# Optimization experiments

Hardware: AMD Instinct MI355X
Metric: run time of the kernel (lower is better)

Reference implementation:

```python
import jax, jax.numpy as jnp
import numpy as np

NUM_HEADS = 16
D_MODEL = 1024
NUM_LAYERS = 4
VOCAB = 32000
SEQ_LEN = 1024
BATCH = 4
EPS = 1e-6


def position_embedding(seq_len, d_model):
    pos = jnp.arange(seq_len, dtype=jnp.float32)[:, None]
    i = jnp.arange(d_model, dtype=jnp.float32)[None, :]
    # faithful to source: angle_rates = 1 / (1/10000)^(2*(i//2)/d) = 10000^(2*(i//2)/d)
    angle_rates = jnp.power(10000.0, 2.0 * jnp.floor(i / 2.0) / float(d_model))
    ang = pos * angle_rates  # [S, D]
    return jnp.concatenate([jnp.sin(ang[:, 0::2]), jnp.cos(ang[:, 1::2])], axis=-1)[None]  # [1,S,D]


def layer_norm(x, g, b):
    m = jnp.mean(x, axis=-1, keepdims=True)
    v = jnp.mean(jnp.square(x - m), axis=-1, keepdims=True)
    return (x - m) * jax.lax.rsqrt(v + EPS) * g + b


def setup_inputs() -> dict:
    key = jax.random.key(0)
    ks = jax.random.split(key, 20)
    L, D = NUM_LAYERS, D_MODEL
    s = 0.02
    inp = {
        "x": jax.random.randint(ks[0], (BATCH, SEQ_LEN), 0, VOCAB, dtype=jnp.int32),
        "mask": jnp.zeros((BATCH, 1, 1, SEQ_LEN), dtype=jnp.float32),
        "emb": jax.random.normal(ks[1], (VOCAB, D), dtype=jnp.float32) * s,
        "wq": jax.random.normal(ks[2], (L, D, D), dtype=jnp.float32) * s,
        "bq": jnp.zeros((L, D), dtype=jnp.float32),
        "wk": jax.random.normal(ks[3], (L, D, D), dtype=jnp.float32) * s,
        "bk": jnp.zeros((L, D), dtype=jnp.float32),
        "wv": jax.random.normal(ks[4], (L, D, D), dtype=jnp.float32) * s,
        "bv": jnp.zeros((L, D), dtype=jnp.float32),
        "wo": jax.random.normal(ks[5], (L, D, D), dtype=jnp.float32) * s,
        "bo": jnp.zeros((L, D), dtype=jnp.float32),
        "wf": jax.random.normal(ks[6], (L, D, D), dtype=jnp.float32) * s,
        "bf": jnp.zeros((L, D), dtype=jnp.float32),
        "g1": jnp.ones((L, D), dtype=jnp.float32),
        "b1": jnp.zeros((L, D), dtype=jnp.float32),
        "g2": jnp.ones((L, D), dtype=jnp.float32),
        "b2": jnp.zeros((L, D), dtype=jnp.float32),
    }
    return inp


def encoder_forward(x, mask, emb, wq, bq, wk, bk, wv, bv, wo, bo, wf, bf, g1, b1, g2, b2):
    B, S = x.shape
    D = emb.shape[1]
    H = NUM_HEADS
    dh = D // H
    h = emb[x] * jnp.sqrt(jnp.float32(D))  # [B,S,D]
    h = h + position_embedding(S, D)[:, :S, :]

    def split_heads(t):  # [B,S,D] -> [B,H,S,dh]
        return t.reshape(B, S, H, dh).transpose(0, 2, 1, 3)

    for l in range(wq.shape[0]):
        q = split_heads(h @ wq[l] + bq[l])
        k = split_heads(h @ wk[l] + bk[l])
        v = split_heads(h @ wv[l] + bv[l])
        scores = jnp.einsum("bhqd,bhkd->bhqk", q, k) / jnp.sqrt(jnp.float32(dh))
        scores = scores + mask * -1e9
        w = jax.nn.softmax(scores, axis=-1)
        ctx = jnp.einsum("bhqk,bhkd->bhqd", w, v)  # [B,H,S,dh]
        ctx = ctx.transpose(0, 2, 1, 3).reshape(B, S, D)
        attn_out = ctx @ wo[l] + bo[l]
        h = layer_norm(h + attn_out, g1[l], b1[l])
        ff = h @ wf[l] + bf[l]
        h = layer_norm(h + ff, g2[l], b2[l])
    return h


def reference(x, mask, emb, wq, bq, wk, bk, wv, bv, wo, bo, wf, bf, g1, b1, g2, b2):
    return encoder_forward(x, mask, emb, wq, bq, wk, bk, wv, bv, wo, bo, wf, bf, g1, b1, g2, b2)
```

## Files before the change

kernel.cpp:

```cpp
#include <hip/hip_runtime.h>
#include <hip/hip_bf16.h>
#include <math.h>

typedef __hip_bfloat16 bf16;
typedef unsigned int u32;
typedef __attribute__((ext_vector_type(8))) short short8;
typedef __attribute__((ext_vector_type(4))) float f32x4;


#define ATT_LDK 72
#define PS_LD  72

typedef __attribute__((address_space(3))) u32 lds_u32;
typedef const __attribute__((address_space(1))) u32 glb_u32;
static __device__ __forceinline__ void g2l16(const void* g, void* l) {
    __builtin_amdgcn_global_load_lds((glb_u32*)g, (lds_u32*)l, 16, 0, 0);
}

static __device__ __forceinline__ unsigned short bf16bits(float f) {
    bf16 h = __float2bfloat16(f);
    return *(unsigned short*)&h;
}

__global__ __launch_bounds__(256) void wprep_kernel(
    const float* __restrict__ wq, const float* __restrict__ wk,
    const float* __restrict__ wv, const float* __restrict__ wo,
    const float* __restrict__ wf, bf16* __restrict__ wt_all)
{
    __shared__ bf16 tile[64][ATT_LDK];
    const int z = blockIdx.z;
    const int l = z / 5, f = z % 5;
    const float* src = (f == 0) ? wq : (f == 1) ? wk : (f == 2) ? wv : (f == 3) ? wo : wf;
    src += (size_t)l * 1024 * 1024;
    bf16* dst = wt_all + ((size_t)l * 5 + f) * 1024 * 1024;

    const int k0 = blockIdx.x * 64, n0 = blockIdx.y * 64;
    const int t = threadIdx.x;
#pragma unroll
    for (int rr = 0; rr < 4; ++rr) {
        int slot = t + rr * 256;
        int r = slot >> 4, c = slot & 15;
        float4 v = *(const float4*)(src + (size_t)(k0 + r) * 1024 + n0 + c * 4);
        tile[c * 4 + 0][r] = __float2bfloat16(v.x);
        tile[c * 4 + 1][r] = __float2bfloat16(v.y);
        tile[c * 4 + 2][r] = __float2bfloat16(v.z);
        tile[c * 4 + 3][r] = __float2bfloat16(v.w);
    }
    __syncthreads();
#pragma unroll
    for (int rr = 0; rr < 2; ++rr) {
        int slot = t + rr * 256;
        int n = slot >> 3, c = slot & 7;
        *(uint4*)(dst + (size_t)(n0 + n) * 1024 + k0 + c * 8) = *(const uint4*)&tile[n][c * 8];
    }
}

__global__ void bias_stack_kernel(const float* __restrict__ bq, const float* __restrict__ bk,
                                  const float* __restrict__ bv, float* __restrict__ bqkv)
{
    int i = blockIdx.x * 256 + threadIdx.x;
    if (i < 4 * 3072) {
        int l = i / 3072, c = i % 3072;
        int fam = c >> 10, cc = c & 1023;
        const float* s = (fam == 0) ? bq : (fam == 1) ? bk : bv;
        bqkv[i] = s[l * 1024 + cc];
    }
}

__global__ __launch_bounds__(256) void pe_kernel(float* __restrict__ pe)
{
    int idx = blockIdx.x * 256 + threadIdx.x;
    int d0 = (idx & 255) * 4;
    int s = idx >> 8;
    float out[4];
#pragma unroll
    for (int j = 0; j < 4; ++j) {
        int d = d0 + j;
        int m = (d < 512) ? d : (d - 512);
        float ex = (float)(2 * m) * (1.0f / 1024.0f);
        float rate = (float)pow(10000.0, (double)ex);
        float ang = (float)s * rate;
        double a = (double)ang;
        out[j] = (d < 512) ? (float)sin(a) : (float)cos(a);
    }
    *(float4*)(pe + (size_t)s * 1024 + d0) = *(float4*)out;
}

__global__ __launch_bounds__(256) void embed_kernel(
    const int* __restrict__ x, const float* __restrict__ emb,
    const float* __restrict__ pe,
    float* __restrict__ hf, bf16* __restrict__ hb)
{
    int idx = blockIdx.x * 256 + threadIdx.x;
    int d0 = (idx & 255) * 4;
    int row = idx >> 8;
    int s = row & 1023;
    int tok = x[row];
    float4 e = *(const float4*)(emb + (size_t)tok * 1024 + d0);
    float4 p = *(const float4*)(pe + (size_t)s * 1024 + d0);
    float out[4] = {e.x * 32.0f + p.x, e.y * 32.0f + p.y,
                    e.z * 32.0f + p.z, e.w * 32.0f + p.w};
    *(float4*)(hf + (size_t)row * 1024 + d0) = *(float4*)out;
    unsigned short pk[4];
#pragma unroll
    for (int j = 0; j < 4; ++j) pk[j] = bf16bits(out[j]);
    *(uint2*)(hb + (size_t)row * 1024 + d0) = *(uint2*)pk;
}

__global__ __launch_bounds__(256, 3) void gemm_bt_kernel(
    const bf16* __restrict__ A, const bf16* __restrict__ Bt,
    const float* __restrict__ bias,
    bf16* __restrict__ Cb, bf16* __restrict__ VtOut,
    int M, int N, int K)
{
    __shared__ bf16 As[128 * 32];
    __shared__ bf16 Bs[128 * 32];
    __shared__ bf16 Cst[4][16 * PS_LD];
    const int t = threadIdx.x;
    const int lane = t & 63, wave = t >> 6;
    const int wr = wave >> 1, wc = wave & 1;
    const int lidx = lane & 15, quad = lane >> 4;
    const int m0 = blockIdx.x * 128, n0 = blockIdx.y * 128;

    f32x4 acc[4][4];
#pragma unroll
    for (int i = 0; i < 4; ++i)
#pragma unroll
        for (int j = 0; j < 4; ++j) acc[i][j] = (f32x4){0.f, 0.f, 0.f, 0.f};

    const int r0 = wave * 32;
    const int rloc = lane >> 2;
    const int csw = ((lane & 3) ^ ((lane >> 3) & 3)) * 8;
    const bf16* Abase = A  + (size_t)(m0 + r0 + rloc) * K + csw;
    const bf16* Bbase = Bt + (size_t)(n0 + r0 + rloc) * K + csw;
    bf16* AsW = As + r0 * 32;
    bf16* BsW = Bs + r0 * 32;
    const int aslot = (quad ^ ((lidx >> 1) & 3)) * 8;

    for (int k0 = 0; k0 < K; k0 += 32) {
        __syncthreads();
        g2l16(Abase + k0,                  AsW);
        g2l16(Abase + k0 + 16 * (size_t)K, AsW + 16 * 32);
        g2l16(Bbase + k0,                  BsW);
        g2l16(Bbase + k0 + 16 * (size_t)K, BsW + 16 * 32);
        __syncthreads();

        short8 af[4], bfr[4];
#pragma unroll
        for (int i = 0; i < 4; ++i)
            af[i] = *(const short8*)(As + (wr * 64 + i * 16 + lidx) * 32 + aslot);
#pragma unroll
        for (int j = 0; j < 4; ++j)
            bfr[j] = *(const short8*)(Bs + (wc * 64 + j * 16 + lidx) * 32 + aslot);
#pragma unroll
        for (int i = 0; i < 4; ++i)
#pragma unroll
            for (int j = 0; j < 4; ++j)
                acc[i][j] = __builtin_amdgcn_mfma_f32_16x16x32_bf16(af[i], bfr[j], acc[i][j], 0, 0, 0);
    }

    float bvj[4];
#pragma unroll
    for (int j = 0; j < 4; ++j)
        bvj[j] = bias ? bias[n0 + wc * 64 + j * 16 + lidx] : 0.0f;

    if (VtOut && n0 >= 2048) {
        const int bidx = m0 >> 10;
        const int s_base = (m0 & 1023) + wr * 64 + quad * 4;
        const int d_base = (n0 - 2048) + wc * 64;
#pragma unroll
        for (int i = 0; i < 4; ++i)
#pragma unroll
            for (int j = 0; j < 4; ++j) {
                unsigned short pk[4];
#pragma unroll
                for (int r = 0; r < 4; ++r)
                    pk[r] = bf16bits(acc[i][j][r] + bvj[j]);
                bf16* dst = VtOut + ((size_t)bidx * 1024 + d_base + j * 16 + lidx) * 1024
                            + s_base + i * 16;
                *(uint2*)dst = *(const uint2*)pk;
            }
    } else {
        const int row16 = lane >> 2, c4 = lane & 3;
#pragma unroll
        for (int i = 0; i < 4; ++i) {
#pragma unroll
            for (int j = 0; j < 4; ++j)
#pragma unroll
                for (int r = 0; r < 4; ++r)
                    Cst[wave][(quad * 4 + r) * PS_LD + j * 16 + lidx] =
                        __float2bfloat16(acc[i][j][r] + bvj[j]);
            bf16* dst = Cb + (size_t)(m0 + wr * 64 + i * 16 + row16) * N + n0 + wc * 64;
            const bf16* srcr = &Cst[wave][row16 * PS_LD];
#pragma unroll
            for (int h = 0; h < 2; ++h)
                *(uint4*)(dst + (c4 + 4 * h) * 8) = *(const uint4*)(srcr + (c4 + 4 * h) * 8);
        }
    }
}

__global__ __launch_bounds__(256, 4) void gemm64_kernel(
    const bf16* __restrict__ A, const bf16* __restrict__ Bt,
    const float* __restrict__ bias, float* __restrict__ Cf,
    int M, int N, int K)
{
    __shared__ bf16 As[64 * 32];
    __shared__ bf16 Bs[128 * 32];
    const int t = threadIdx.x;
    const int lane = t & 63, wave = t >> 6;
    const int wr = wave >> 1, wc = wave & 1;
    const int lidx = lane & 15, quad = lane >> 4;
    const int m0 = blockIdx.x * 64, n0 = blockIdx.y * 128;

    f32x4 acc[2][4];
#pragma unroll
    for (int i = 0; i < 2; ++i)
#pragma unroll
        for (int j = 0; j < 4; ++j) acc[i][j] = (f32x4){0.f, 0.f, 0.f, 0.f};

    const int rloc = lane >> 2;
    const int csw = ((lane & 3) ^ ((lane >> 3) & 3)) * 8;
    const bf16* Abase = A  + (size_t)(m0 + wave * 16 + rloc) * K + csw;
    const bf16* Bbase = Bt + (size_t)(n0 + wave * 32 + rloc) * K + csw;
    bf16* AsW = As + wave * 16 * 32;
    bf16* BsW = Bs + wave * 32 * 32;
    const int aslot = (quad ^ ((lidx >> 1) & 3)) * 8;

    for (int k0 = 0; k0 < K; k0 += 32) {
        __syncthreads();
        g2l16(Abase + k0,                  AsW);
        g2l16(Bbase + k0,                  BsW);
        g2l16(Bbase + k0 + 16 * (size_t)K, BsW + 16 * 32);
        __syncthreads();

        short8 af[2], bfr[4];
#pragma unroll
        for (int i = 0; i < 2; ++i)
            af[i] = *(const short8*)(As + (wr * 32 + i * 16 + lidx) * 32 + aslot);
#pragma unroll
        for (int j = 0; j < 4; ++j)
            bfr[j] = *(const short8*)(Bs + (wc * 64 + j * 16 + lidx) * 32 + aslot);
#pragma unroll
        for (int i = 0; i < 2; ++i)
#pragma unroll
            for (int j = 0; j < 4; ++j)
                acc[i][j] = __builtin_amdgcn_mfma_f32_16x16x32_bf16(af[i], bfr[j], acc[i][j], 0, 0, 0);
    }

#pragma unroll
    for (int i = 0; i < 2; ++i)
#pragma unroll
        for (int j = 0; j < 4; ++j) {
            int col = n0 + wc * 64 + j * 16 + lidx;
            float bv = bias[col];
#pragma unroll
            for (int r = 0; r < 4; ++r) {
                int rowg = m0 + wr * 32 + i * 16 + quad * 4 + r;
                Cf[(size_t)rowg * N + col] = acc[i][j][r] + bv;
            }
        }
}

__global__ __launch_bounds__(512, 4) void attention_kernel(
    const bf16* __restrict__ QKV,
    const bf16* __restrict__ Vt,
    const float* __restrict__ mask,
    bf16* __restrict__ ctx)
{
    __shared__ bf16 Ks[64 * 64];
    __shared__ bf16 Vs[64 * 64];
    __shared__ bf16 Ps[8][16 * PS_LD];

    const int t = threadIdx.x, lane = t & 63, wave = t >> 6;
    const int quad = lane >> 4, lidx = lane & 15;
    const int b = blockIdx.x >> 4, hh = blockIdx.x & 15;
    const int q0 = blockIdx.y * 128 + wave * 16;

    const int r8 = lane >> 3;
    const int gc = ((lane & 7) ^ r8) * 8;
    const bf16* kg0 = QKV + (size_t)(b * 1024 + wave * 8 + r8) * 3072 + 1024 + hh * 64 + gc;
    const bf16* vg0 = Vt  + (size_t)(b * 1024 + hh * 64 + wave * 8 + r8) * 1024 + gc;
    bf16* KsW = Ks + wave * 8 * 64;
    bf16* VsW = Vs + wave * 8 * 64;

    short8 qf[2];
    {
        const bf16* qp = QKV + (size_t)(b * 1024 + q0 + lidx) * 3072 + hh * 64;
        qf[0] = *(const short8*)(qp + quad * 8);
        qf[1] = *(const short8*)(qp + 32 + quad * 8);
    }

    f32x4 Oacc[4];
#pragma unroll
    for (int nt = 0; nt < 4; ++nt) Oacc[nt] = (f32x4){0.f, 0.f, 0.f, 0.f};
    float psum[4] = {0.f, 0.f, 0.f, 0.f};

    const int fslot = lidx & 7;

    for (int kt = 0; kt < 16; ++kt) {
        __syncthreads();
        g2l16(kg0 + (size_t)kt * 64 * 3072, KsW);
        g2l16(vg0 + kt * 64, VsW);
        __syncthreads();

        f32x4 sacc[4];
#pragma unroll
        for (int nt = 0; nt < 4; ++nt) sacc[nt] = (f32x4){0.f, 0.f, 0.f, 0.f};
#pragma unroll
        for (int kk = 0; kk < 2; ++kk)
#pragma unroll
            for (int nt = 0; nt < 4; ++nt) {
                short8 kf = *(const short8*)(Ks + (nt * 16 + lidx) * 64 + (((kk * 4 + quad) ^ fslot) * 8));
                sacc[nt] = __builtin_amdgcn_mfma_f32_16x16x32_bf16(qf[kk], kf, sacc[nt], 0, 0, 0);
            }

#pragma unroll
        for (int nt = 0; nt < 4; ++nt) {
            float mv = mask[b * 1024 + kt * 64 + nt * 16 + lidx] * -1e9f;
#pragma unroll
            for (int r = 0; r < 4; ++r) {
                float p = __expf(sacc[nt][r] * 0.125f + mv);
                sacc[nt][r] = p;
                psum[r] += p;
            }
        }

#pragma unroll
        for (int nt = 0; nt < 4; ++nt)
#pragma unroll
            for (int r = 0; r < 4; ++r)
                Ps[wave][(quad * 4 + r) * PS_LD + nt * 16 + lidx] = __float2bfloat16(sacc[nt][r]);

#pragma unroll
        for (int kk = 0; kk < 2; ++kk) {
            short8 pf = *(const short8*)(&Ps[wave][lidx * PS_LD + kk * 32 + quad * 8]);
#pragma unroll
            for (int nt = 0; nt < 4; ++nt) {
                short8 vf = *(const short8*)(Vs + (nt * 16 + lidx) * 64 + (((kk * 4 + quad) ^ fslot) * 8));
                Oacc[nt] = __builtin_amdgcn_mfma_f32_16x16x32_bf16(pf, vf, Oacc[nt], 0, 0, 0);
            }
        }
    }

#pragma unroll
    for (int off = 1; off < 16; off <<= 1)
#pragma unroll
        for (int r = 0; r < 4; ++r)
            psum[r] += __shfl_xor(psum[r], off, 64);
    float linv[4];
#pragma unroll
    for (int r = 0; r < 4; ++r) linv[r] = 1.0f / psum[r];

#pragma unroll
    for (int nt = 0; nt < 4; ++nt)
#pragma unroll
        for (int r = 0; r < 4; ++r)
            Ps[wave][(quad * 4 + r) * PS_LD + nt * 16 + lidx] = __float2bfloat16(Oacc[nt][r] * linv[r]);

    const int row16 = lane >> 2, c4 = lane & 3;
    bf16* dst = ctx + (size_t)(b * 1024 + q0 + row16) * 1024 + hh * 64;
    const bf16* srcr = &Ps[wave][row16 * PS_LD];
#pragma unroll
    for (int h = 0; h < 2; ++h)
        *(uint4*)(dst + (c4 + 4 * h) * 8) = *(const uint4*)(srcr + (c4 + 4 * h) * 8);
}

__global__ __launch_bounds__(256) void add_ln_kernel(
    const float* __restrict__ x, const float* __restrict__ dx,
    const float* __restrict__ g, const float* __restrict__ b,
    float* __restrict__ outf, bf16* __restrict__ outb)
{
    __shared__ float red[4];
    const int row = blockIdx.x;
    const int t = threadIdx.x;
    const int c0 = t * 4;
    float4 xv = *(const float4*)(x + (size_t)row * 1024 + c0);
    float4 dv = *(const float4*)(dx + (size_t)row * 1024 + c0);
    float v[4] = {xv.x + dv.x, xv.y + dv.y, xv.z + dv.z, xv.w + dv.w};
    float s = v[0] + v[1] + v[2] + v[3];
#pragma unroll
    for (int off = 1; off < 64; off <<= 1) s += __shfl_xor(s, off, 64);
    if ((t & 63) == 0) red[t >> 6] = s;
    __syncthreads();
    float mean = (red[0] + red[1] + red[2] + red[3]) * (1.0f / 1024.0f);
    float sq = 0.f;
#pragma unroll
    for (int i = 0; i < 4; ++i) { float d = v[i] - mean; sq += d * d; }
#pragma unroll
    for (int off = 1; off < 64; off <<= 1) sq += __shfl_xor(sq, off, 64);
    __syncthreads();
    if ((t & 63) == 0) red[t >> 6] = sq;
    __syncthreads();
    float var = (red[0] + red[1] + red[2] + red[3]) * (1.0f / 1024.0f);
    float rs = rsqrtf(var + 1e-6f);
    float4 gv = *(const float4*)(g + c0);
    float4 bv = *(const float4*)(b + c0);
    float gg[4] = {gv.x, gv.y, gv.z, gv.w}, bb[4] = {bv.x, bv.y, bv.z, bv.w};
    float o[4];
    unsigned short pk[4];
#pragma unroll
    for (int i = 0; i < 4; ++i) {
        o[i] = (v[i] - mean) * rs * gg[i] + bb[i];
        pk[i] = bf16bits(o[i]);
    }
    *(float4*)(outf + (size_t)row * 1024 + c0) = *(float4*)o;
    *(uint2*)(outb + (size_t)row * 1024 + c0) = *(uint2*)pk;
}

extern "C" void kernel_launch(void* const* d_in, const int* in_sizes, int n_in,
                              void* d_out, int out_size, void* d_ws, size_t ws_size,
                              hipStream_t stream)
{
    const int*   x    = (const int*)d_in[0];
    const float* mask = (const float*)d_in[1];
    const float* emb  = (const float*)d_in[2];
    const float* wq   = (const float*)d_in[3];
    const float* bq   = (const float*)d_in[4];
    const float* wk   = (const float*)d_in[5];
    const float* bk   = (const float*)d_in[6];
    const float* wv   = (const float*)d_in[7];
    const float* bv   = (const float*)d_in[8];
    const float* wo   = (const float*)d_in[9];
    const float* bo   = (const float*)d_in[10];
    const float* wf   = (const float*)d_in[11];
    const float* bfp  = (const float*)d_in[12];
    const float* g1   = (const float*)d_in[13];
    const float* b1   = (const float*)d_in[14];
    const float* g2   = (const float*)d_in[15];
    const float* b2   = (const float*)d_in[16];

    char* ws = (char*)d_ws;
    float* h_f  = (float*)ws;                 ws += 4096ull * 1024 * 4;
    bf16*  h_b  = (bf16*)ws;                  ws += 4096ull * 1024 * 2;
    bf16*  qkv  = (bf16*)ws;                  ws += 4096ull * 3072 * 2;
    bf16*  vt   = (bf16*)ws;                  ws += 4096ull * 1024 * 2;
    bf16*  ctx  = (bf16*)ws;                  ws += 4096ull * 1024 * 2;
    bf16*  wt   = (bf16*)ws;                  ws += 20ull * 1024 * 1024 * 2;
    float* pe   = (float*)ws;                 ws += 1024ull * 1024 * 4;
    float* bqkv = (float*)ws;                 ws += 4ull * 3072 * 4;
    float* delta = (float*)qkv;

    wprep_kernel<<<dim3(16, 16, 20), 256, 0, stream>>>(wq, wk, wv, wo, wf, wt);
    bias_stack_kernel<<<dim3(48), 256, 0, stream>>>(bq, bk, bv, bqkv);
    pe_kernel<<<dim3(1024), 256, 0, stream>>>(pe);
    embed_kernel<<<dim3(4096), 256, 0, stream>>>(x, emb, pe, h_f, h_b);

    for (int l = 0; l < 4; ++l) {
        bf16* wt_l = wt + (size_t)l * 5 * 1024 * 1024;
        gemm_bt_kernel<<<dim3(32, 24), 256, 0, stream>>>(
            h_b, wt_l, bqkv + l * 3072, qkv, vt, 4096, 3072, 1024);
        attention_kernel<<<dim3(64, 8), 512, 0, stream>>>(qkv, vt, mask, ctx);
        gemm64_kernel<<<dim3(64, 8), 256, 0, stream>>>(
            ctx, wt_l + 3ull * 1024 * 1024, bo + l * 1024, delta, 4096, 1024, 1024);
        add_ln_kernel<<<dim3(4096), 256, 0, stream>>>(
            h_f, delta, g1 + l * 1024, b1 + l * 1024, h_f, h_b);
        gemm64_kernel<<<dim3(64, 8), 256, 0, stream>>>(
            h_b, wt_l + 4ull * 1024 * 1024, bfp + l * 1024, delta, 4096, 1024, 1024);
        float* outf = (l == 3) ? (float*)d_out : h_f;
        add_ln_kernel<<<dim3(4096), 256, 0, stream>>>(
            h_f, delta, g2 + l * 1024, b2 + l * 1024, outf, h_b);
    }
    (void)in_sizes; (void)n_in; (void)out_size; (void)ws_size;
}
```

Before: 779.7 us.

## Double-buffer LDS tiles in GEMM and attention; fuse residual add into GEMM epilogue

The QKV GEMM, the output/FFN GEMMs and the attention kernel now keep two LDS buffers. Each iteration issues the async global-to-LDS loads for the next K tile, then computes on the current one, which halves the barriers per iteration and overlaps loads with MFMA work. Separately, gemm64 now adds the residual in its epilogue, so add_ln only reads one input. The extra LDS may lower how many attention blocks fit on a CU, and the overlap window is still closed by the barrier at the top of the next iteration.

```diff
diff --git a/kernel.cpp b/kernel.cpp
--- a/kernel.cpp
+++ b/kernel.cpp
@@ -113,8 +113,8 @@
     bf16* __restrict__ Cb, bf16* __restrict__ VtOut,
     int M, int N, int K)
 {
-    __shared__ bf16 As[128 * 32];
-    __shared__ bf16 Bs[128 * 32];
+    __shared__ bf16 As[2][128 * 32];
+    __shared__ bf16 Bs[2][128 * 32];
     __shared__ bf16 Cst[4][16 * PS_LD];
     const int t = threadIdx.x;
     const int lane = t & 63, wave = t >> 6;
@@ -133,25 +133,32 @@
     const int csw = ((lane & 3) ^ ((lane >> 3) & 3)) * 8;
     const bf16* Abase = A  + (size_t)(m0 + r0 + rloc) * K + csw;
     const bf16* Bbase = Bt + (size_t)(n0 + r0 + rloc) * K + csw;
-    bf16* AsW = As + r0 * 32;
-    bf16* BsW = Bs + r0 * 32;
+    const int lofs = r0 * 32;
     const int aslot = (quad ^ ((lidx >> 1) & 3)) * 8;
+
+    g2l16(Abase,                  &As[0][lofs]);
+    g2l16(Abase + 16 * (size_t)K, &As[0][lofs + 16 * 32]);
+    g2l16(Bbase,                  &Bs[0][lofs]);
+    g2l16(Bbase + 16 * (size_t)K, &Bs[0][lofs + 16 * 32]);
 
     for (int k0 = 0; k0 < K; k0 += 32) {
         __syncthreads();
-        g2l16(Abase + k0,                  AsW);
-        g2l16(Abase + k0 + 16 * (size_t)K, AsW + 16 * 32);
-        g2l16(Bbase + k0,                  BsW);
-        g2l16(Bbase + k0 + 16 * (size_t)K, BsW + 16 * 32);
-        __syncthreads();
+        const int cur = (k0 >> 5) & 1;
+        if (k0 + 32 < K) {
+            const int kn = k0 + 32;
+            g2l16(Abase + kn,                  &As[cur ^ 1][lofs]);
+            g2l16(Abase + kn + 16 * (size_t)K, &As[cur ^ 1][lofs + 16 * 32]);
+            g2l16(Bbase + kn,                  &Bs[cur ^ 1][lofs]);
+            g2l16(Bbase + kn + 16 * (size_t)K, &Bs[cur ^ 1][lofs + 16 * 32]);
+        }
 
         short8 af[4], bfr[4];
 #pragma unroll
         for (int i = 0; i < 4; ++i)
-            af[i] = *(const short8*)(As + (wr * 64 + i * 16 + lidx) * 32 + aslot);
+            af[i] = *(const short8*)(&As[cur][(wr * 64 + i * 16 + lidx) * 32 + aslot]);
 #pragma unroll
         for (int j = 0; j < 4; ++j)
-            bfr[j] = *(const short8*)(Bs + (wc * 64 + j * 16 + lidx) * 32 + aslot);
+            bfr[j] = *(const short8*)(&Bs[cur][(wc * 64 + j * 16 + lidx) * 32 + aslot]);
 #pragma unroll
         for (int i = 0; i < 4; ++i)
 #pragma unroll
@@ -201,11 +208,12 @@
 
 __global__ __launch_bounds__(256, 4) void gemm64_kernel(
     const bf16* __restrict__ A, const bf16* __restrict__ Bt,
-    const float* __restrict__ bias, float* __restrict__ Cf,
+    const float* __restrict__ bias, const float* __restrict__ resid,
+    float* __restrict__ Cf,
     int M, int N, int K)
 {
-    __shared__ bf16 As[64 * 32];
-    __shared__ bf16 Bs[128 * 32];
+    __shared__ bf16 As[2][64 * 32];
+    __shared__ bf16 Bs[2][128 * 32];
     const int t = threadIdx.x;
     const int lane = t & 63, wave = t >> 6;
     const int wr = wave >> 1, wc = wave & 1;
@@ -222,24 +230,31 @@
     const int csw = ((lane & 3) ^ ((lane >> 3) & 3)) * 8;
     const bf16* Abase = A  + (size_t)(m0 + wave * 16 + rloc) * K + csw;
     const bf16* Bbase = Bt + (size_t)(n0 + wave * 32 + rloc) * K + csw;
-    bf16* AsW = As + wave * 16 * 32;
-    bf16* BsW = Bs + wave * 32 * 32;
+    const int alofs = wave * 16 * 32;
+    const int blofs = wave * 32 * 32;
     const int aslot = (quad ^ ((lidx >> 1) & 3)) * 8;
+
+    g2l16(Abase,                  &As[0][alofs]);
+    g2l16(Bbase,                  &Bs[0][blofs]);
+    g2l16(Bbase + 16 * (size_t)K, &Bs[0][blofs + 16 * 32]);
 
     for (int k0 = 0; k0 < K; k0 += 32) {
         __syncthreads();
-        g2l16(Abase + k0,                  AsW);
-        g2l16(Bbase + k0,                  BsW);
-        g2l16(Bbase + k0 + 16 * (size_t)K, BsW + 16 * 32);
-        __syncthreads();
+        const int cur = (k0 >> 5) & 1;
+        if (k0 + 32 < K) {
+            const int kn = k0 + 32;
+            g2l16(Abase + kn,                  &As[cur ^ 1][alofs]);
+            g2l16(Bbase + kn,                  &Bs[cur ^ 1][blofs]);
+            g2l16(Bbase + kn + 16 * (size_t)K, &Bs[cur ^ 1][blofs + 16 * 32]);
+        }
 
         short8 af[2], bfr[4];
 #pragma unroll
         for (int i = 0; i < 2; ++i)
-            af[i] = *(const short8*)(As + (wr * 32 + i * 16 + lidx) * 32 + aslot);
+            af[i] = *(const short8*)(&As[cur][(wr * 32 + i * 16 + lidx) * 32 + aslot]);
 #pragma unroll
         for (int j = 0; j < 4; ++j)
-            bfr[j] = *(const short8*)(Bs + (wc * 64 + j * 16 + lidx) * 32 + aslot);
+            bfr[j] = *(const short8*)(&Bs[cur][(wc * 64 + j * 16 + lidx) * 32 + aslot]);
 #pragma unroll
         for (int i = 0; i < 2; ++i)
 #pragma unroll
@@ -256,7 +271,8 @@
 #pragma unroll
             for (int r = 0; r < 4; ++r) {
                 int rowg = m0 + wr * 32 + i * 16 + quad * 4 + r;
-                Cf[(size_t)rowg * N + col] = acc[i][j][r] + bv;
+                Cf[(size_t)rowg * N + col] =
+                    acc[i][j][r] + bv + resid[(size_t)rowg * N + col];
             }
         }
 }
@@ -267,8 +283,8 @@
     const float* __restrict__ mask,
     bf16* __restrict__ ctx)
 {
-    __shared__ bf16 Ks[64 * 64];
-    __shared__ bf16 Vs[64 * 64];
+    __shared__ bf16 Ks[2][64 * 64];
+    __shared__ bf16 Vs[2][64 * 64];
     __shared__ bf16 Ps[8][16 * PS_LD];
 
     const int t = threadIdx.x, lane = t & 63, wave = t >> 6;
@@ -280,8 +296,7 @@
     const int gc = ((lane & 7) ^ r8) * 8;
     const bf16* kg0 = QKV + (size_t)(b * 1024 + wave * 8 + r8) * 3072 + 1024 + hh * 64 + gc;
     const bf16* vg0 = Vt  + (size_t)(b * 1024 + hh * 64 + wave * 8 + r8) * 1024 + gc;
-    bf16* KsW = Ks + wave * 8 * 64;
-    bf16* VsW = Vs + wave * 8 * 64;
+    const int lofs = wave * 8 * 64;
 
     short8 qf[2];
     {
@@ -297,11 +312,16 @@
 
     const int fslot = lidx & 7;
 
+    g2l16(kg0, &Ks[0][lofs]);
+    g2l16(vg0, &Vs[0][lofs]);
+
     for (int kt = 0; kt < 16; ++kt) {
         __syncthreads();
-        g2l16(kg0 + (size_t)kt * 64 * 3072, KsW);
-        g2l16(vg0 + kt * 64, VsW);
-        __syncthreads();
+        const int cur = kt & 1;
+        if (kt < 15) {
+            g2l16(kg0 + (size_t)(kt + 1) * 64 * 3072, &Ks[cur ^ 1][lofs]);
+            g2l16(vg0 + (kt + 1) * 64,                &Vs[cur ^ 1][lofs]);
+        }
 
         f32x4 sacc[4];
 #pragma unroll
@@ -310,7 +330,7 @@
         for (int kk = 0; kk < 2; ++kk)
 #pragma unroll
             for (int nt = 0; nt < 4; ++nt) {
-                short8 kf = *(const short8*)(Ks + (nt * 16 + lidx) * 64 + (((kk * 4 + quad) ^ fslot) * 8));
+                short8 kf = *(const short8*)(&Ks[cur][(nt * 16 + lidx) * 64 + (((kk * 4 + quad) ^ fslot) * 8)]);
                 sacc[nt] = __builtin_amdgcn_mfma_f32_16x16x32_bf16(qf[kk], kf, sacc[nt], 0, 0, 0);
             }
 
@@ -336,7 +356,7 @@
             short8 pf = *(const short8*)(&Ps[wave][lidx * PS_LD + kk * 32 + quad * 8]);
 #pragma unroll
             for (int nt = 0; nt < 4; ++nt) {
-                short8 vf = *(const short8*)(Vs + (nt * 16 + lidx) * 64 + (((kk * 4 + quad) ^ fslot) * 8));
+                short8 vf = *(const short8*)(&Vs[cur][(nt * 16 + lidx) * 64 + (((kk * 4 + quad) ^ fslot) * 8)]);
                 Oacc[nt] = __builtin_amdgcn_mfma_f32_16x16x32_bf16(pf, vf, Oacc[nt], 0, 0, 0);
             }
         }
@@ -366,7 +386,7 @@
 }
 
 __global__ __launch_bounds__(256) void add_ln_kernel(
-    const float* __restrict__ x, const float* __restrict__ dx,
+    const float* __restrict__ x,
     const float* __restrict__ g, const float* __restrict__ b,
     float* __restrict__ outf, bf16* __restrict__ outb)
 {
@@ -375,8 +395,7 @@
     const int t = threadIdx.x;
     const int c0 = t * 4;
     float4 xv = *(const float4*)(x + (size_t)row * 1024 + c0);
-    float4 dv = *(const float4*)(dx + (size_t)row * 1024 + c0);
-    float v[4] = {xv.x + dv.x, xv.y + dv.y, xv.z + dv.z, xv.w + dv.w};
+    float v[4] = {xv.x, xv.y, xv.z, xv.w};
     float s = v[0] + v[1] + v[2] + v[3];
 #pragma unroll
     for (int off = 1; off < 64; off <<= 1) s += __shfl_xor(s, off, 64);
@@ -451,14 +470,14 @@
             h_b, wt_l, bqkv + l * 3072, qkv, vt, 4096, 3072, 1024);
         attention_kernel<<<dim3(64, 8), 512, 0, stream>>>(qkv, vt, mask, ctx);
         gemm64_kernel<<<dim3(64, 8), 256, 0, stream>>>(
-            ctx, wt_l + 3ull * 1024 * 1024, bo + l * 1024, delta, 4096, 1024, 1024);
+            ctx, wt_l + 3ull * 1024 * 1024, bo + l * 1024, h_f, delta, 4096, 1024, 1024);
         add_ln_kernel<<<dim3(4096), 256, 0, stream>>>(
-            h_f, delta, g1 + l * 1024, b1 + l * 1024, h_f, h_b);
+            delta, g1 + l * 1024, b1 + l * 1024, h_f, h_b);
         gemm64_kernel<<<dim3(64, 8), 256, 0, stream>>>(
-            h_b, wt_l + 4ull * 1024 * 1024, bfp + l * 1024, delta, 4096, 1024, 1024);
+            h_b, wt_l + 4ull * 1024 * 1024, bfp + l * 1024, h_f, delta, 4096, 1024, 1024);
         float* outf = (l == 3) ? (float*)d_out : h_f;
         add_ln_kernel<<<dim3(4096), 256, 0, stream>>>(
-            h_f, delta, g2 + l * 1024, b2 + l * 1024, outf, h_b);
+            delta, g2 + l * 1024, b2 + l * 1024, outf, h_b);
     }
     (void)in_sizes; (void)n_in; (void)out_size; (void)ws_size;
 }
```

After: 774.9 us. Within noise of the previous version (-0.6%).
